# Kernel tuning notes

Hardware: AMD Instinct MI355X
Metric: run time of the kernel (lower is better)

The kernel has to match this reference:

```python
import jax, jax.numpy as jnp
import numpy as np

H = 20  # hidden_size


def _cell(x, h, c, Wih, Whh, b):
    # PyTorch LSTM gate order: i, f, g, o ; b = b_ih + b_hh (merged)
    g = x @ Wih.T + h @ Whh.T + b
    i, f, gg, o = jnp.split(g, 4, axis=-1)
    c = jax.nn.sigmoid(f) * c + jax.nn.sigmoid(i) * jnp.tanh(gg)
    h = jax.nn.sigmoid(o) * jnp.tanh(c)
    return h, c


def _run_lstm(seq, h0, c0, params):
    # seq: [B,T,D]; h0,c0: [L,B,H]; params: list of (Wih, Whh, b) per layer
    def step(carry, x_t):
        h, c = carry
        inp = x_t
        hs, cs = [], []
        for l, (Wih, Whh, b) in enumerate(params):
            hl, cl = _cell(inp, h[l], c[l], Wih, Whh, b)
            hs.append(hl); cs.append(cl)
            inp = hl
        h = jnp.stack(hs); c = jnp.stack(cs)
        return (h, c), h[-1]
    (h, c), last_layer_h = jax.lax.scan(step, (h0, c0), jnp.swapaxes(seq, 0, 1))
    return h, c, last_layer_h  # last_layer_h: [T,B,H]


def setup_inputs() -> dict:
    key = jax.random.key(0)
    ks = jax.random.split(key, 32)
    B = 131072
    d = {
        'y_past': jax.random.normal(ks[0], (B, 8, 1), jnp.float32),
        'x_past': jax.random.normal(ks[1], (B, 8, 8), jnp.float32),
        'u_past': jax.random.normal(ks[2], (B, 8, 4), jnp.float32),
        's_past': jax.random.normal(ks[3], (B, 8, 3), jnp.float32),
        'u_future': jax.random.normal(ks[4], (B, 4, 4), jnp.float32),
    }
    s = 0.1
    # lstm (input_size=16), 2 layers
    d['Wih1_0'] = jax.random.normal(ks[5], (4 * H, 16), jnp.float32) * s
    d['Whh1_0'] = jax.random.normal(ks[6], (4 * H, H), jnp.float32) * s
    d['b1_0'] = jax.random.normal(ks[7], (4 * H,), jnp.float32) * s
    d['Wih1_1'] = jax.random.normal(ks[8], (4 * H, H), jnp.float32) * s
    d['Whh1_1'] = jax.random.normal(ks[9], (4 * H, H), jnp.float32) * s
    d['b1_1'] = jax.random.normal(ks[10], (4 * H,), jnp.float32) * s
    # lstm_2 (input_size=u_size=4), 2 layers
    d['Wih2_0'] = jax.random.normal(ks[11], (4 * H, 4), jnp.float32) * s
    d['Whh2_0'] = jax.random.normal(ks[12], (4 * H, H), jnp.float32) * s
    d['b2_0'] = jax.random.normal(ks[13], (4 * H,), jnp.float32) * s
    d['Wih2_1'] = jax.random.normal(ks[14], (4 * H, H), jnp.float32) * s
    d['Whh2_1'] = jax.random.normal(ks[15], (4 * H, H), jnp.float32) * s
    d['b2_1'] = jax.random.normal(ks[16], (4 * H,), jnp.float32) * s
    # FCNN 20 -> 10 -> 10 -> 1
    d['fW1'] = jax.random.normal(ks[17], (10, 20), jnp.float32) * s
    d['fb1'] = jax.random.normal(ks[18], (10,), jnp.float32) * s
    d['fW2'] = jax.random.normal(ks[19], (10, 10), jnp.float32) * s
    d['fb2'] = jax.random.normal(ks[20], (10,), jnp.float32) * s
    d['fW3'] = jax.random.normal(ks[21], (1, 10), jnp.float32) * s
    d['fb3'] = jax.random.normal(ks[22], (1,), jnp.float32) * s
    return d


def reference(y_past, x_past, u_past, s_past, u_future,
              Wih1_0, Whh1_0, b1_0, Wih1_1, Whh1_1, b1_1,
              Wih2_0, Whh2_0, b2_0, Wih2_1, Whh2_1, b2_1,
              fW1, fb1, fW2, fb2, fW3, fb3):
    inp = jnp.concatenate([y_past, x_past, u_past, s_past], axis=2)  # [B,T,16]
    B = inp.shape[0]
    h0 = jnp.zeros((2, B, H), inp.dtype)
    c0 = jnp.zeros((2, B, H), inp.dtype)
    # encoder LSTM over lookback window (state carried, outputs discarded)
    h, c, _ = _run_lstm(inp, h0, c0, [(Wih1_0, Whh1_0, b1_0), (Wih1_1, Whh1_1, b1_1)])
    # decoder LSTM over lookahead, collecting last-layer h each step
    _, _, hs = _run_lstm(u_future, h, c, [(Wih2_0, Whh2_0, b2_0), (Wih2_1, Whh2_1, b2_1)])
    # FCNN head applied per step: [T2,B,H] -> [T2,B,1]
    z = jax.nn.relu(hs @ fW1.T + fb1)
    z = jax.nn.relu(z @ fW2.T + fb2)
    z = z @ fW3.T + fb3
    return jnp.swapaxes(z, 0, 1)  # [B, lookahead, 1]
```

## Files before the change

### kernel.cpp

```cpp
#include <hip/hip_runtime.h>
#include <utility>

#define HH 20

typedef float v2f __attribute__((ext_vector_type(2)));

__device__ __forceinline__ float fast_rcp(float x) { return __builtin_amdgcn_rcpf(x); }
__device__ __forceinline__ float fsigmoid(float x) { return fast_rcp(1.0f + __expf(-x)); }
__device__ __forceinline__ float ftanh(float x) {
    float e = __expf(2.0f * x);
    return 1.0f - 2.0f * fast_rcp(e + 1.0f);
}
__device__ __forceinline__ float pswap(float v) {
    return __int_as_float(__builtin_amdgcn_mov_dpp(__float_as_int(v), 0xB1, 0xF, 0xF, true));
}
__device__ __forceinline__ v2f fma2(v2f a, v2f b, v2f c) {
#if __has_builtin(__builtin_elementwise_fma)
    return __builtin_elementwise_fma(a, b, c);
#else
    v2f r; r.x = fmaf(a.x, b.x, c.x); r.y = fmaf(a.y, b.y, c.y); return r;
#endif
}

constexpr int BLK16 = 20 * 16 + 4;
constexpr int BLK20 = 20 * 20 + 4;
constexpr int BLK4  = 20 * 4 + 4;

constexpr int W_Wih1_0 = 0;
constexpr int W_Whh1_0 = W_Wih1_0 + 4 * BLK16;
constexpr int W_b1_0   = W_Whh1_0 + 4 * BLK20;
constexpr int W_Wih1_1 = W_b1_0 + 80;
constexpr int W_Whh1_1 = W_Wih1_1 + 4 * BLK20;
constexpr int W_b1_1   = W_Whh1_1 + 4 * BLK20;
constexpr int W_Wih2_0 = W_b1_1 + 80;
constexpr int W_Whh2_0 = W_Wih2_0 + 4 * BLK4;
constexpr int W_b2_0   = W_Whh2_0 + 4 * BLK20;
constexpr int W_Wih2_1 = W_b2_0 + 80;
constexpr int W_Whh2_1 = W_Wih2_1 + 4 * BLK20;
constexpr int W_b2_1   = W_Whh2_1 + 4 * BLK20;
constexpr int W_fW1    = W_b2_1 + 80;
constexpr int W_fb1    = W_fW1 + 200;
constexpr int W_fW2    = W_fb1 + 12;
constexpr int W_fb2    = W_fW2 + 100;
constexpr int W_fW3    = W_fb2 + 12;
constexpr int W_fb3    = W_fW3 + 10;
constexpr int LDS_TOT  = W_fb3 + 2;

template <int IN, size_t U, size_t K>
__device__ __forceinline__ void row2_k(const float (&sm)[LDS_TOT], int rb,
                                       const v2f (&v)[IN], v2f& a) {
    float4 w = *(const float4*)&sm[rb + (int)(U * IN + 4 * K)];
    v2f w0 = {w.x, w.x}, w1 = {w.y, w.y}, w2 = {w.z, w.z}, w3 = {w.w, w.w};
    a = fma2(w0, v[4 * K + 0], a);
    a = fma2(w1, v[4 * K + 1], a);
    a = fma2(w2, v[4 * K + 2], a);
    a = fma2(w3, v[4 * K + 3], a);
}
template <int IN, size_t U, size_t... K>
__device__ __forceinline__ void row2(const float (&sm)[LDS_TOT], int rb,
                                     const v2f (&v)[IN], v2f& a, std::index_sequence<K...>) {
    (row2_k<IN, U, K>(sm, rb, v, a), ...);
}

template <int IN, size_t U>
__device__ __forceinline__ void unit2(const float (&sm)[LDS_TOT], int s, float m, float mm1,
                                      int wihA, int wihB, int whhA, int whhB, int bA, int bB,
                                      const v2f (&xp)[IN], const v2f (&hp)[HH],
                                      float (&c_own)[HH], float (&hn)[HH]) {
    float bAv = sm[bA + (int)U];
    float bBv = sm[bB + (int)U];
    v2f aA = {bAv, bAv};
    v2f aB = {bBv, bBv};
    row2<IN, U>(sm, wihA, xp, aA, std::make_index_sequence<IN / 4>{});
    row2<IN, U>(sm, wihB, xp, aB, std::make_index_sequence<IN / 4>{});
    row2<HH, U>(sm, whhA, hp, aA, std::make_index_sequence<HH / 4>{});
    row2<HH, U>(sm, whhB, hp, aB, std::make_index_sequence<HH / 4>{});
    float Ao = fsigmoid(aA.x), At = fsigmoid(aA.y);
    float Bo = fmaf(m, fsigmoid(m * aB.x), -mm1);
    float Bt = fmaf(m, fsigmoid(m * aB.y), -mm1);
    float rA = pswap(At);
    float rB = pswap(Bt);
    float sf = s ? rB : Bo;
    float si = s ? rA : Ao;
    float tg = s ? Bo : rB;
    float so = s ? Ao : rA;
    float cn = fmaf(sf, c_own[U], si * tg);
    c_own[U] = cn;
    hn[U] = so * ftanh(cn);
}

template <int WIH, int WHH, int BOFF, int IN, int BLK, size_t... U, size_t... K>
__device__ __forceinline__ void cell_impl(const float (&sm)[LDS_TOT], int wb, int s,
                                          float m, float mm1,
                                          const float (&x_own)[IN],
                                          float (&h_own)[HH], float (&c_own)[HH],
                                          std::index_sequence<U...>, std::index_sequence<K...>) {
    v2f xp[IN], hp[HH];
    ((xp[K].x = x_own[K], xp[K].y = pswap(x_own[K])), ...);
    ((hp[U].x = h_own[U], hp[U].y = pswap(h_own[U])), ...);
    const int gA = s ? 3 : 0, gB = s ? 2 : 1;
    int wihA = wb + WIH + gA * BLK;
    int wihB = wb + WIH + gB * BLK;
    int whhA = wb + WHH + gA * BLK20;
    int whhB = wb + WHH + gB * BLK20;
    int bA = wb + BOFF + gA * 20;
    int bB = wb + BOFF + gB * 20;
    float hn[HH];
    (unit2<IN, U>(sm, s, m, mm1, wihA, wihB, whhA, whhB, bA, bB,
                  xp, hp, c_own, hn), ...);
    ((h_own[U] = hn[U]), ...);
}

template <int WIH, int WHH, int BOFF, int IN, int BLK>
__device__ __forceinline__ void cell(const float (&sm)[LDS_TOT], int wb, int s,
                                     float m, float mm1, const float (&x_own)[IN],
                                     float (&h_own)[HH], float (&c_own)[HH]) {
    cell_impl<WIH, WHH, BOFF, IN, BLK>(sm, wb, s, m, mm1, x_own, h_own, c_own,
                                       std::make_index_sequence<HH>{},
                                       std::make_index_sequence<IN>{});
}

template <int WOFF, size_t J, int LD, int NV, size_t... K>
__device__ __forceinline__ float mlp_dot(const float (&sm)[LDS_TOT], int wb, const float (&v)[NV],
                                         float a, std::index_sequence<K...>) {
    ((a = fmaf(sm[wb + WOFF + (int)(J * LD + K)], v[K], a)), ...);
    return a;
}
template <size_t... J>
__device__ __forceinline__ void mlp_l1(const float (&sm)[LDS_TOT], int wb,
                                       const float (&h)[HH], float (&z)[10], std::index_sequence<J...>) {
    ((z[J] = fmaxf(mlp_dot<W_fW1, J, HH>(sm, wb, h, sm[wb + W_fb1 + (int)J],
                                         std::make_index_sequence<HH>{}), 0.f)), ...);
}
template <size_t... J>
__device__ __forceinline__ void mlp_l2(const float (&sm)[LDS_TOT], int wb,
                                       const float (&z1)[10], float (&z2)[10], std::index_sequence<J...>) {
    ((z2[J] = fmaxf(mlp_dot<W_fW2, J, 10>(sm, wb, z1, sm[wb + W_fb2 + (int)J],
                                          std::make_index_sequence<10>{}), 0.f)), ...);
}

__global__ void __launch_bounds__(256, 2) lstm_ar_kernel(
    const float* __restrict__ y_past, const float* __restrict__ x_past,
    const float* __restrict__ u_past, const float* __restrict__ s_past,
    const float* __restrict__ u_future,
    const float* __restrict__ Wih1_0, const float* __restrict__ Whh1_0, const float* __restrict__ b1_0,
    const float* __restrict__ Wih1_1, const float* __restrict__ Whh1_1, const float* __restrict__ b1_1,
    const float* __restrict__ Wih2_0, const float* __restrict__ Whh2_0, const float* __restrict__ b2_0,
    const float* __restrict__ Wih2_1, const float* __restrict__ Whh2_1, const float* __restrict__ b2_1,
    const float* __restrict__ fW1, const float* __restrict__ fb1,
    const float* __restrict__ fW2, const float* __restrict__ fb2,
    const float* __restrict__ fW3, const float* __restrict__ fb3,
    float* __restrict__ out, int B) {
    __shared__ __align__(16) float smem[LDS_TOT];
    const int tid = threadIdx.x;

    auto stage_w = [&](const float* src, int off, int IN) {
        const int gb = 20 * IN;
        for (int i = tid; i < 4 * gb; i += 256) {
            int g = i / gb;
            smem[off + g * (gb + 4) + (i - g * gb)] = src[i];
        }
    };
    auto stage = [&](const float* src, int off, int n) {
        for (int i = tid; i < n; i += 256) smem[off + i] = src[i];
    };
    stage_w(Wih1_0, W_Wih1_0, 16);
    stage_w(Whh1_0, W_Whh1_0, 20);
    stage(b1_0, W_b1_0, 80);
    stage_w(Wih1_1, W_Wih1_1, 20);
    stage_w(Whh1_1, W_Whh1_1, 20);
    stage(b1_1, W_b1_1, 80);
    stage_w(Wih2_0, W_Wih2_0, 4);
    stage_w(Whh2_0, W_Whh2_0, 20);
    stage(b2_0, W_b2_0, 80);
    stage_w(Wih2_1, W_Wih2_1, 20);
    stage_w(Whh2_1, W_Whh2_1, 20);
    stage(b2_1, W_b2_1, 80);
    stage(fW1, W_fW1, 200);
    stage(fb1, W_fb1, 10);
    stage(fW2, W_fW2, 100);
    stage(fb2, W_fb2, 10);
    stage(fW3, W_fW3, 10);
    stage(fb3, W_fb3, 1);
    __syncthreads();

    const int s = tid & 1;
    const int e = blockIdx.x * 256 + tid;
    if (e >= B) return;

    const float m   = s ? 2.0f : 1.0f;
    const float mm1 = m - 1.0f;

    float h0[HH], c0[HH], h1[HH], c1[HH];
    {
        auto zero = [&](auto... u) {
            ((h0[u] = 0.f, c0[u] = 0.f, h1[u] = 0.f, c1[u] = 0.f), ...);
        };
        zero(0, 1, 2, 3, 4, 5, 6, 7, 8, 9, 10, 11, 12, 13, 14, 15, 16, 17, 18, 19);
    }

    int wb = 0;

#pragma clang loop unroll(disable)
    for (int t = 0; t < 8; ++t) {
        asm volatile("" : "+s"(wb));
        float x[16];
        x[0] = y_past[e * 8 + t];
        {
            const float4* p = (const float4*)(x_past + (size_t)(e * 8 + t) * 8);
            float4 a0 = p[0], a1 = p[1];
            x[1] = a0.x; x[2] = a0.y; x[3] = a0.z; x[4] = a0.w;
            x[5] = a1.x; x[6] = a1.y; x[7] = a1.z; x[8] = a1.w;
        }
        {
            const float4* p = (const float4*)(u_past + (size_t)(e * 8 + t) * 4);
            float4 a0 = p[0];
            x[9] = a0.x; x[10] = a0.y; x[11] = a0.z; x[12] = a0.w;
        }
        {
            const float* p = s_past + (size_t)(e * 8 + t) * 3;
            x[13] = p[0]; x[14] = p[1]; x[15] = p[2];
        }
        cell<W_Wih1_0, W_Whh1_0, W_b1_0, 16, BLK16>(smem, wb, s, m, mm1, x, h0, c0);
        cell<W_Wih1_1, W_Whh1_1, W_b1_1, HH, BLK20>(smem, wb, s, m, mm1, h0, h1, c1);
    }

#pragma clang loop unroll(disable)
    for (int t = 0; t < 4; ++t) {
        asm volatile("" : "+s"(wb));
        float x[4];
        {
            const float4* p = (const float4*)(u_future + (size_t)(e * 4 + t) * 4);
            float4 a0 = p[0];
            x[0] = a0.x; x[1] = a0.y; x[2] = a0.z; x[3] = a0.w;
        }
        cell<W_Wih2_0, W_Whh2_0, W_b2_0, 4, BLK4>(smem, wb, s, m, mm1, x, h0, c0);
        cell<W_Wih2_1, W_Whh2_1, W_b2_1, HH, BLK20>(smem, wb, s, m, mm1, h0, h1, c1);

        float z1[10], z2[10];
        mlp_l1(smem, wb, h1, z1, std::make_index_sequence<10>{});
        mlp_l2(smem, wb, z1, z2, std::make_index_sequence<10>{});
        float o = mlp_dot<W_fW3, 0, 10>(smem, wb, z2, smem[wb + W_fb3],
                                        std::make_index_sequence<10>{});
        out[e * 4 + t] = o;
    }
}

extern "C" void kernel_launch(void* const* d_in, const int* in_sizes, int n_in,
                              void* d_out, int out_size, void* d_ws, size_t ws_size,
                              hipStream_t stream) {
    (void)n_in; (void)d_ws; (void)ws_size;
    const float* y_past   = (const float*)d_in[0];
    const float* x_past   = (const float*)d_in[1];
    const float* u_past   = (const float*)d_in[2];
    const float* s_past   = (const float*)d_in[3];
    const float* u_future = (const float*)d_in[4];
    const float* Wih1_0 = (const float*)d_in[5];
    const float* Whh1_0 = (const float*)d_in[6];
    const float* b1_0   = (const float*)d_in[7];
    const float* Wih1_1 = (const float*)d_in[8];
    const float* Whh1_1 = (const float*)d_in[9];
    const float* b1_1   = (const float*)d_in[10];
    const float* Wih2_0 = (const float*)d_in[11];
    const float* Whh2_0 = (const float*)d_in[12];
    const float* b2_0   = (const float*)d_in[13];
    const float* Wih2_1 = (const float*)d_in[14];
    const float* Whh2_1 = (const float*)d_in[15];
    const float* b2_1   = (const float*)d_in[16];
    const float* fW1 = (const float*)d_in[17];
    const float* fb1 = (const float*)d_in[18];
    const float* fW2 = (const float*)d_in[19];
    const float* fb2 = (const float*)d_in[20];
    const float* fW3 = (const float*)d_in[21];
    const float* fb3 = (const float*)d_in[22];
    float* out = (float*)d_out;

    int B = in_sizes[0] / 8;
    (void)out_size;

    dim3 block(256);
    dim3 grid((B + 255) / 256);
    lstm_ar_kernel<<<grid, block, 0, stream>>>(
        y_past, x_past, u_past, s_past, u_future,
        Wih1_0, Whh1_0, b1_0, Wih1_1, Whh1_1, b1_1,
        Wih2_0, Whh2_0, b2_0, Wih2_1, Whh2_1, b2_1,
        fW1, fb1, fW2, fb2, fW3, fb3, out, B);
}
```

Measured before the change: 562.6 us.

## Read LSTM weights from global scalar loads instead of LDS with lane-pair split

Drops LDS staging of all weights and the lane-pair scheme where two adjacent threads split gate work via DPP swaps. Each thread now computes all four gates for its own batch element, loading weights straight from global memory at wave-uniform addresses that the compiler can issue as scalar loads. Dot products use packed pairs along the input dimension, reduced at the end. This removes LDS traffic and cross-lane shuffles but doubles per-thread gate arithmetic and depends on scalar cache bandwidth.

Measured after the change: 855.5 us. 1.52x slower.

```diff
diff --git a/kernel.cpp b/kernel.cpp
--- a/kernel.cpp
+++ b/kernel.cpp
@@ -11,9 +11,7 @@
     float e = __expf(2.0f * x);
     return 1.0f - 2.0f * fast_rcp(e + 1.0f);
 }
-__device__ __forceinline__ float pswap(float v) {
-    return __int_as_float(__builtin_amdgcn_mov_dpp(__float_as_int(v), 0xB1, 0xF, 0xF, true));
-}
+
 __device__ __forceinline__ v2f fma2(v2f a, v2f b, v2f c) {
 #if __has_builtin(__builtin_elementwise_fma)
     return __builtin_elementwise_fma(a, b, c);
@@ -22,121 +20,87 @@
 #endif
 }
 
-constexpr int BLK16 = 20 * 16 + 4;
-constexpr int BLK20 = 20 * 20 + 4;
-constexpr int BLK4  = 20 * 4 + 4;
-
-constexpr int W_Wih1_0 = 0;
-constexpr int W_Whh1_0 = W_Wih1_0 + 4 * BLK16;
-constexpr int W_b1_0   = W_Whh1_0 + 4 * BLK20;
-constexpr int W_Wih1_1 = W_b1_0 + 80;
-constexpr int W_Whh1_1 = W_Wih1_1 + 4 * BLK20;
-constexpr int W_b1_1   = W_Whh1_1 + 4 * BLK20;
-constexpr int W_Wih2_0 = W_b1_1 + 80;
-constexpr int W_Whh2_0 = W_Wih2_0 + 4 * BLK4;
-constexpr int W_b2_0   = W_Whh2_0 + 4 * BLK20;
-constexpr int W_Wih2_1 = W_b2_0 + 80;
-constexpr int W_Whh2_1 = W_Wih2_1 + 4 * BLK20;
-constexpr int W_b2_1   = W_Whh2_1 + 4 * BLK20;
-constexpr int W_fW1    = W_b2_1 + 80;
-constexpr int W_fb1    = W_fW1 + 200;
-constexpr int W_fW2    = W_fb1 + 12;
-constexpr int W_fb2    = W_fW2 + 100;
-constexpr int W_fW3    = W_fb2 + 12;
-constexpr int W_fb3    = W_fW3 + 10;
-constexpr int LDS_TOT  = W_fb3 + 2;
-
-template <int IN, size_t U, size_t K>
-__device__ __forceinline__ void row2_k(const float (&sm)[LDS_TOT], int rb,
-                                       const v2f (&v)[IN], v2f& a) {
-    float4 w = *(const float4*)&sm[rb + (int)(U * IN + 4 * K)];
-    v2f w0 = {w.x, w.x}, w1 = {w.y, w.y}, w2 = {w.z, w.z}, w3 = {w.w, w.w};
-    a = fma2(w0, v[4 * K + 0], a);
-    a = fma2(w1, v[4 * K + 1], a);
-    a = fma2(w2, v[4 * K + 2], a);
-    a = fma2(w3, v[4 * K + 3], a);
-}
-template <int IN, size_t U, size_t... K>
-__device__ __forceinline__ void row2(const float (&sm)[LDS_TOT], int rb,
-                                     const v2f (&v)[IN], v2f& a, std::index_sequence<K...>) {
-    (row2_k<IN, U, K>(sm, rb, v, a), ...);
-}
-
-template <int IN, size_t U>
-__device__ __forceinline__ void unit2(const float (&sm)[LDS_TOT], int s, float m, float mm1,
-                                      int wihA, int wihB, int whhA, int whhB, int bA, int bB,
-                                      const v2f (&xp)[IN], const v2f (&hp)[HH],
-                                      float (&c_own)[HH], float (&hn)[HH]) {
-    float bAv = sm[bA + (int)U];
-    float bBv = sm[bB + (int)U];
-    v2f aA = {bAv, bAv};
-    v2f aB = {bBv, bBv};
-    row2<IN, U>(sm, wihA, xp, aA, std::make_index_sequence<IN / 4>{});
-    row2<IN, U>(sm, wihB, xp, aB, std::make_index_sequence<IN / 4>{});
-    row2<HH, U>(sm, whhA, hp, aA, std::make_index_sequence<HH / 4>{});
-    row2<HH, U>(sm, whhB, hp, aB, std::make_index_sequence<HH / 4>{});
-    float Ao = fsigmoid(aA.x), At = fsigmoid(aA.y);
-    float Bo = fmaf(m, fsigmoid(m * aB.x), -mm1);
-    float Bt = fmaf(m, fsigmoid(m * aB.y), -mm1);
-    float rA = pswap(At);
-    float rB = pswap(Bt);
-    float sf = s ? rB : Bo;
-    float si = s ? rA : Ao;
-    float tg = s ? Bo : rB;
-    float so = s ? Ao : rA;
-    float cn = fmaf(sf, c_own[U], si * tg);
-    c_own[U] = cn;
+template <int NP, size_t... J>
+__device__ __forceinline__ v2f dot2i(const float* __restrict__ W, int base,
+                                     const v2f (&p)[NP], v2f acc, std::index_sequence<J...>) {
+    ((acc = fma2(*(const v2f*)(W + base + 2 * (int)J), p[J], acc)), ...);
+    return acc;
+}
+template <int NP>
+__device__ __forceinline__ v2f dot2(const float* __restrict__ W, int base,
+                                    const v2f (&p)[NP], v2f acc) {
+    return dot2i<NP>(W, base, p, acc, std::make_index_sequence<NP>{});
+}
+
+template <int N, size_t... J>
+__device__ __forceinline__ void mkpairs_i(const float (&a)[N], v2f (&p)[N / 2],
+                                          std::index_sequence<J...>) {
+    ((p[J] = v2f{a[2 * J], a[2 * J + 1]}), ...);
+}
+template <int N>
+__device__ __forceinline__ void mkpairs(const float (&a)[N], v2f (&p)[N / 2]) {
+    mkpairs_i<N>(a, p, std::make_index_sequence<N / 2>{});
+}
+
+template <int IN, int U>
+__device__ __forceinline__ void unitK(const float* __restrict__ Wih, const float* __restrict__ Whh,
+                                      const float* __restrict__ bb, int z,
+                                      const v2f (&xp)[IN / 2], const v2f (&hp)[HH / 2],
+                                      float (&c)[HH], float (&hn)[HH]) {
+    const v2f zz = {0.f, 0.f};
+    v2f ai = dot2<IN / 2>(Wih, z + (0 * HH + U) * IN, xp, zz);
+    v2f af = dot2<IN / 2>(Wih, z + (1 * HH + U) * IN, xp, zz);
+    v2f ag = dot2<IN / 2>(Wih, z + (2 * HH + U) * IN, xp, zz);
+    v2f ao = dot2<IN / 2>(Wih, z + (3 * HH + U) * IN, xp, zz);
+    ai = dot2<HH / 2>(Whh, z + (0 * HH + U) * HH, hp, ai);
+    af = dot2<HH / 2>(Whh, z + (1 * HH + U) * HH, hp, af);
+    ag = dot2<HH / 2>(Whh, z + (2 * HH + U) * HH, hp, ag);
+    ao = dot2<HH / 2>(Whh, z + (3 * HH + U) * HH, hp, ao);
+    float gi = ai.x + ai.y + bb[z + 0 * HH + U];
+    float gf = af.x + af.y + bb[z + 1 * HH + U];
+    float gg = ag.x + ag.y + bb[z + 2 * HH + U];
+    float go = ao.x + ao.y + bb[z + 3 * HH + U];
+    float si = fsigmoid(gi);
+    float sf = fsigmoid(gf);
+    float so = fsigmoid(go);
+    float tg = ftanh(gg);
+    float cn = fmaf(sf, c[U], si * tg);
+    c[U] = cn;
     hn[U] = so * ftanh(cn);
 }
 
-template <int WIH, int WHH, int BOFF, int IN, int BLK, size_t... U, size_t... K>
-__device__ __forceinline__ void cell_impl(const float (&sm)[LDS_TOT], int wb, int s,
-                                          float m, float mm1,
-                                          const float (&x_own)[IN],
-                                          float (&h_own)[HH], float (&c_own)[HH],
-                                          std::index_sequence<U...>, std::index_sequence<K...>) {
-    v2f xp[IN], hp[HH];
-    ((xp[K].x = x_own[K], xp[K].y = pswap(x_own[K])), ...);
-    ((hp[U].x = h_own[U], hp[U].y = pswap(h_own[U])), ...);
-    const int gA = s ? 3 : 0, gB = s ? 2 : 1;
-    int wihA = wb + WIH + gA * BLK;
-    int wihB = wb + WIH + gB * BLK;
-    int whhA = wb + WHH + gA * BLK20;
-    int whhB = wb + WHH + gB * BLK20;
-    int bA = wb + BOFF + gA * 20;
-    int bB = wb + BOFF + gB * 20;
+template <int IN, size_t... U>
+__device__ __forceinline__ void cellK_u(const float* __restrict__ Wih, const float* __restrict__ Whh,
+                                        const float* __restrict__ bb, int z,
+                                        const v2f (&xp)[IN / 2], float (&h)[HH], float (&c)[HH],
+                                        std::index_sequence<U...>) {
+    v2f hp[HH / 2];
+    mkpairs<HH>(h, hp);
     float hn[HH];
-    (unit2<IN, U>(sm, s, m, mm1, wihA, wihB, whhA, whhB, bA, bB,
-                  xp, hp, c_own, hn), ...);
-    ((h_own[U] = hn[U]), ...);
-}
-
-template <int WIH, int WHH, int BOFF, int IN, int BLK>
-__device__ __forceinline__ void cell(const float (&sm)[LDS_TOT], int wb, int s,
-                                     float m, float mm1, const float (&x_own)[IN],
-                                     float (&h_own)[HH], float (&c_own)[HH]) {
-    cell_impl<WIH, WHH, BOFF, IN, BLK>(sm, wb, s, m, mm1, x_own, h_own, c_own,
-                                       std::make_index_sequence<HH>{},
-                                       std::make_index_sequence<IN>{});
-}
-
-template <int WOFF, size_t J, int LD, int NV, size_t... K>
-__device__ __forceinline__ float mlp_dot(const float (&sm)[LDS_TOT], int wb, const float (&v)[NV],
-                                         float a, std::index_sequence<K...>) {
-    ((a = fmaf(sm[wb + WOFF + (int)(J * LD + K)], v[K], a)), ...);
-    return a;
-}
-template <size_t... J>
-__device__ __forceinline__ void mlp_l1(const float (&sm)[LDS_TOT], int wb,
-                                       const float (&h)[HH], float (&z)[10], std::index_sequence<J...>) {
-    ((z[J] = fmaxf(mlp_dot<W_fW1, J, HH>(sm, wb, h, sm[wb + W_fb1 + (int)J],
-                                         std::make_index_sequence<HH>{}), 0.f)), ...);
-}
-template <size_t... J>
-__device__ __forceinline__ void mlp_l2(const float (&sm)[LDS_TOT], int wb,
-                                       const float (&z1)[10], float (&z2)[10], std::index_sequence<J...>) {
-    ((z2[J] = fmaxf(mlp_dot<W_fW2, J, 10>(sm, wb, z1, sm[wb + W_fb2 + (int)J],
-                                          std::make_index_sequence<10>{}), 0.f)), ...);
+    (unitK<IN, (int)U>(Wih, Whh, bb, z, xp, hp, c, hn), ...);
+    ((h[U] = hn[U]), ...);
+}
+template <int IN>
+__device__ __forceinline__ void cellK(const float* __restrict__ Wih, const float* __restrict__ Whh,
+                                      const float* __restrict__ bb, int z,
+                                      const float (&x)[IN], float (&h)[HH], float (&c)[HH]) {
+    v2f xp[IN / 2];
+    mkpairs<IN>(x, xp);
+    cellK_u<IN>(Wih, Whh, bb, z, xp, h, c, std::make_index_sequence<HH>{});
+}
+
+template <int NP>
+__device__ __forceinline__ float rowdot(const float* __restrict__ W, int base,
+                                        const v2f (&p)[NP], float b) {
+    const v2f zz = {0.f, 0.f};
+    v2f a = dot2<NP>(W, base, p, zz);
+    return a.x + a.y + b;
+}
+template <int NP, int LD, size_t... J>
+__device__ __forceinline__ void mlp_layer(const float* __restrict__ W, const float* __restrict__ bv,
+                                          int z, const v2f (&p)[NP], float (&o)[10],
+                                          std::index_sequence<J...>) {
+    ((o[J] = fmaxf(rowdot<NP>(W, z + (int)J * LD, p, bv[z + (int)J]), 0.f)), ...);
 }
 
 __global__ void __launch_bounds__(256, 2) lstm_ar_kernel(
@@ -151,45 +115,8 @@
     const float* __restrict__ fW2, const float* __restrict__ fb2,
     const float* __restrict__ fW3, const float* __restrict__ fb3,
     float* __restrict__ out, int B) {
-    __shared__ __align__(16) float smem[LDS_TOT];
-    const int tid = threadIdx.x;
-
-    auto stage_w = [&](const float* src, int off, int IN) {
-        const int gb = 20 * IN;
-        for (int i = tid; i < 4 * gb; i += 256) {
-            int g = i / gb;
-            smem[off + g * (gb + 4) + (i - g * gb)] = src[i];
-        }
-    };
-    auto stage = [&](const float* src, int off, int n) {
-        for (int i = tid; i < n; i += 256) smem[off + i] = src[i];
-    };
-    stage_w(Wih1_0, W_Wih1_0, 16);
-    stage_w(Whh1_0, W_Whh1_0, 20);
-    stage(b1_0, W_b1_0, 80);
-    stage_w(Wih1_1, W_Wih1_1, 20);
-    stage_w(Whh1_1, W_Whh1_1, 20);
-    stage(b1_1, W_b1_1, 80);
-    stage_w(Wih2_0, W_Wih2_0, 4);
-    stage_w(Whh2_0, W_Whh2_0, 20);
-    stage(b2_0, W_b2_0, 80);
-    stage_w(Wih2_1, W_Wih2_1, 20);
-    stage_w(Whh2_1, W_Whh2_1, 20);
-    stage(b2_1, W_b2_1, 80);
-    stage(fW1, W_fW1, 200);
-    stage(fb1, W_fb1, 10);
-    stage(fW2, W_fW2, 100);
-    stage(fb2, W_fb2, 10);
-    stage(fW3, W_fW3, 10);
-    stage(fb3, W_fb3, 1);
-    __syncthreads();
-
-    const int s = tid & 1;
-    const int e = blockIdx.x * 256 + tid;
+    const int e = blockIdx.x * 256 + threadIdx.x;
     if (e >= B) return;
-
-    const float m   = s ? 2.0f : 1.0f;
-    const float mm1 = m - 1.0f;
 
     float h0[HH], c0[HH], h1[HH], c1[HH];
     {
@@ -199,11 +126,10 @@
         zero(0, 1, 2, 3, 4, 5, 6, 7, 8, 9, 10, 11, 12, 13, 14, 15, 16, 17, 18, 19);
     }
 
-    int wb = 0;
-
 #pragma clang loop unroll(disable)
     for (int t = 0; t < 8; ++t) {
-        asm volatile("" : "+s"(wb));
+        int z = 0;
+        asm volatile("" : "+s"(z));
         float x[16];
         x[0] = y_past[e * 8 + t];
         {
@@ -221,27 +147,33 @@
             const float* p = s_past + (size_t)(e * 8 + t) * 3;
             x[13] = p[0]; x[14] = p[1]; x[15] = p[2];
         }
-        cell<W_Wih1_0, W_Whh1_0, W_b1_0, 16, BLK16>(smem, wb, s, m, mm1, x, h0, c0);
-        cell<W_Wih1_1, W_Whh1_1, W_b1_1, HH, BLK20>(smem, wb, s, m, mm1, h0, h1, c1);
+        cellK<16>(Wih1_0, Whh1_0, b1_0, z, x, h0, c0);
+        cellK<HH>(Wih1_1, Whh1_1, b1_1, z, h0, h1, c1);
     }
 
 #pragma clang loop unroll(disable)
     for (int t = 0; t < 4; ++t) {
-        asm volatile("" : "+s"(wb));
+        int z = 0;
+        asm volatile("" : "+s"(z));
         float x[4];
         {
             const float4* p = (const float4*)(u_future + (size_t)(e * 4 + t) * 4);
             float4 a0 = p[0];
             x[0] = a0.x; x[1] = a0.y; x[2] = a0.z; x[3] = a0.w;
         }
-        cell<W_Wih2_0, W_Whh2_0, W_b2_0, 4, BLK4>(smem, wb, s, m, mm1, x, h0, c0);
-        cell<W_Wih2_1, W_Whh2_1, W_b2_1, HH, BLK20>(smem, wb, s, m, mm1, h0, h1, c1);
-
+        cellK<4>(Wih2_0, Whh2_0, b2_0, z, x, h0, c0);
+        cellK<HH>(Wih2_1, Whh2_1, b2_1, z, h0, h1, c1);
+
+        v2f hp1[HH / 2];
+        mkpairs<HH>(h1, hp1);
         float z1[10], z2[10];
-        mlp_l1(smem, wb, h1, z1, std::make_index_sequence<10>{});
-        mlp_l2(smem, wb, z1, z2, std::make_index_sequence<10>{});
-        float o = mlp_dot<W_fW3, 0, 10>(smem, wb, z2, smem[wb + W_fb3],
-                                        std::make_index_sequence<10>{});
+        mlp_layer<HH / 2, HH>(fW1, fb1, z, hp1, z1, std::make_index_sequence<10>{});
+        v2f zp1[5];
+        mkpairs<10>(z1, zp1);
+        mlp_layer<5, 10>(fW2, fb2, z, zp1, z2, std::make_index_sequence<10>{});
+        v2f zp2[5];
+        mkpairs<10>(z2, zp2);
+        float o = rowdot<5>(fW3, z + 0, zp2, fb3[z + 0]);
         out[e * 4 + t] = o;
     }
 }
```

## Process two batch elements per thread to reuse LDS weight loads

Applied to the files above, without the earlier changes.

Each thread now carries two independent sequences (e0 and e0+B/2) packed in v2f registers, so every LDS weight load feeds twice as many packed FMAs. The MLP head is also rewritten to use packed fma2 over both elements. The aim is to halve LDS weight traffic per element and improve ILP. In exchange register pressure roughly doubles, the launch bound drops to 128 threads with 1 block per CU, and half as many threads are launched, which lowers occupancy and latency hiding. Odd B would drop the last element.

New measurement: 631.1 us. +12.2%, slower.

```diff
diff --git a/kernel.cpp b/kernel.cpp
--- a/kernel.cpp
+++ b/kernel.cpp
@@ -21,6 +21,8 @@
     v2f r; r.x = fmaf(a.x, b.x, c.x); r.y = fmaf(a.y, b.y, c.y); return r;
 #endif
 }
+__device__ __forceinline__ v2f splat2(float w) { return v2f{w, w}; }
+__device__ __forceinline__ v2f relu2(v2f a) { return v2f{fmaxf(a.x, 0.f), fmaxf(a.y, 0.f)}; }
 
 constexpr int BLK16 = 20 * 16 + 4;
 constexpr int BLK20 = 20 * 20 + 4;
@@ -47,57 +49,78 @@
 constexpr int LDS_TOT  = W_fb3 + 2;
 
 template <int IN, size_t U, size_t K>
-__device__ __forceinline__ void row2_k(const float (&sm)[LDS_TOT], int rb,
-                                       const v2f (&v)[IN], v2f& a) {
+__device__ __forceinline__ void row2x_k(const float (&sm)[LDS_TOT], int rb,
+                                        const v2f (&p0)[IN], const v2f (&p1)[IN],
+                                        v2f& a0, v2f& a1) {
     float4 w = *(const float4*)&sm[rb + (int)(U * IN + 4 * K)];
-    v2f w0 = {w.x, w.x}, w1 = {w.y, w.y}, w2 = {w.z, w.z}, w3 = {w.w, w.w};
-    a = fma2(w0, v[4 * K + 0], a);
-    a = fma2(w1, v[4 * K + 1], a);
-    a = fma2(w2, v[4 * K + 2], a);
-    a = fma2(w3, v[4 * K + 3], a);
+    v2f w0 = splat2(w.x), w1 = splat2(w.y), w2 = splat2(w.z), w3 = splat2(w.w);
+    a0 = fma2(w0, p0[4 * K + 0], a0);  a1 = fma2(w0, p1[4 * K + 0], a1);
+    a0 = fma2(w1, p0[4 * K + 1], a0);  a1 = fma2(w1, p1[4 * K + 1], a1);
+    a0 = fma2(w2, p0[4 * K + 2], a0);  a1 = fma2(w2, p1[4 * K + 2], a1);
+    a0 = fma2(w3, p0[4 * K + 3], a0);  a1 = fma2(w3, p1[4 * K + 3], a1);
 }
 template <int IN, size_t U, size_t... K>
-__device__ __forceinline__ void row2(const float (&sm)[LDS_TOT], int rb,
-                                     const v2f (&v)[IN], v2f& a, std::index_sequence<K...>) {
-    (row2_k<IN, U, K>(sm, rb, v, a), ...);
+__device__ __forceinline__ void row2x(const float (&sm)[LDS_TOT], int rb,
+                                      const v2f (&p0)[IN], const v2f (&p1)[IN],
+                                      v2f& a0, v2f& a1, std::index_sequence<K...>) {
+    (row2x_k<IN, U, K>(sm, rb, p0, p1, a0, a1), ...);
 }
 
 template <int IN, size_t U>
-__device__ __forceinline__ void unit2(const float (&sm)[LDS_TOT], int s, float m, float mm1,
-                                      int wihA, int wihB, int whhA, int whhB, int bA, int bB,
-                                      const v2f (&xp)[IN], const v2f (&hp)[HH],
-                                      float (&c_own)[HH], float (&hn)[HH]) {
+__device__ __forceinline__ void unit2x(const float (&sm)[LDS_TOT], int s, float m, float mm1,
+                                       int wihA, int wihB, int whhA, int whhB, int bA, int bB,
+                                       const v2f (&xp0)[IN], const v2f (&xp1)[IN],
+                                       const v2f (&hp0)[HH], const v2f (&hp1)[HH],
+                                       v2f (&c_own)[HH], v2f (&hn)[HH]) {
     float bAv = sm[bA + (int)U];
     float bBv = sm[bB + (int)U];
-    v2f aA = {bAv, bAv};
-    v2f aB = {bBv, bBv};
-    row2<IN, U>(sm, wihA, xp, aA, std::make_index_sequence<IN / 4>{});
-    row2<IN, U>(sm, wihB, xp, aB, std::make_index_sequence<IN / 4>{});
-    row2<HH, U>(sm, whhA, hp, aA, std::make_index_sequence<HH / 4>{});
-    row2<HH, U>(sm, whhB, hp, aB, std::make_index_sequence<HH / 4>{});
-    float Ao = fsigmoid(aA.x), At = fsigmoid(aA.y);
-    float Bo = fmaf(m, fsigmoid(m * aB.x), -mm1);
-    float Bt = fmaf(m, fsigmoid(m * aB.y), -mm1);
-    float rA = pswap(At);
-    float rB = pswap(Bt);
-    float sf = s ? rB : Bo;
-    float si = s ? rA : Ao;
-    float tg = s ? Bo : rB;
-    float so = s ? Ao : rA;
-    float cn = fmaf(sf, c_own[U], si * tg);
-    c_own[U] = cn;
-    hn[U] = so * ftanh(cn);
+    v2f aA0 = splat2(bAv), aA1 = splat2(bAv);
+    v2f aB0 = splat2(bBv), aB1 = splat2(bBv);
+    row2x<IN, U>(sm, wihA, xp0, xp1, aA0, aA1, std::make_index_sequence<IN / 4>{});
+    row2x<IN, U>(sm, wihB, xp0, xp1, aB0, aB1, std::make_index_sequence<IN / 4>{});
+    row2x<HH, U>(sm, whhA, hp0, hp1, aA0, aA1, std::make_index_sequence<HH / 4>{});
+    row2x<HH, U>(sm, whhB, hp0, hp1, aB0, aB1, std::make_index_sequence<HH / 4>{});
+    float cn0, cn1;
+    {
+        float Ao = fsigmoid(aA0.x), At = fsigmoid(aA0.y);
+        float Bo = fmaf(m, fsigmoid(m * aB0.x), -mm1);
+        float Bt = fmaf(m, fsigmoid(m * aB0.y), -mm1);
+        float rA = pswap(At);
+        float rB = pswap(Bt);
+        float sf = s ? rB : Bo;
+        float si = s ? rA : Ao;
+        float tg = s ? Bo : rB;
+        float so = s ? Ao : rA;
+        cn0 = fmaf(sf, c_own[U].x, si * tg);
+        hn[U].x = so * ftanh(cn0);
+    }
+    {
+        float Ao = fsigmoid(aA1.x), At = fsigmoid(aA1.y);
+        float Bo = fmaf(m, fsigmoid(m * aB1.x), -mm1);
+        float Bt = fmaf(m, fsigmoid(m * aB1.y), -mm1);
+        float rA = pswap(At);
+        float rB = pswap(Bt);
+        float sf = s ? rB : Bo;
+        float si = s ? rA : Ao;
+        float tg = s ? Bo : rB;
+        float so = s ? Ao : rA;
+        cn1 = fmaf(sf, c_own[U].y, si * tg);
+        hn[U].y = so * ftanh(cn1);
+    }
+    c_own[U] = v2f{cn0, cn1};
 }
 
 template <int WIH, int WHH, int BOFF, int IN, int BLK, size_t... U, size_t... K>
 __device__ __forceinline__ void cell_impl(const float (&sm)[LDS_TOT], int wb, int s,
                                           float m, float mm1,
-                                          const float (&x_own)[IN],
-                                          float (&h_own)[HH], float (&c_own)[HH],
+                                          const v2f (&xo)[IN],
+                                          v2f (&h_own)[HH], v2f (&c_own)[HH],
                                           std::index_sequence<U...>, std::index_sequence<K...>) {
-    v2f xp[IN], hp[HH];
-    ((xp[K].x = x_own[K], xp[K].y = pswap(x_own[K])), ...);
-    ((hp[U].x = h_own[U], hp[U].y = pswap(h_own[U])), ...);
+    v2f xp0[IN], xp1[IN], hp0[HH], hp1[HH];
+    ((xp0[K] = v2f{xo[K].x, pswap(xo[K].x)},
+      xp1[K] = v2f{xo[K].y, pswap(xo[K].y)}), ...);
+    ((hp0[U] = v2f{h_own[U].x, pswap(h_own[U].x)},
+      hp1[U] = v2f{h_own[U].y, pswap(h_own[U].y)}), ...);
     const int gA = s ? 3 : 0, gB = s ? 2 : 1;
     int wihA = wb + WIH + gA * BLK;
     int wihB = wb + WIH + gB * BLK;
@@ -105,41 +128,41 @@
     int whhB = wb + WHH + gB * BLK20;
     int bA = wb + BOFF + gA * 20;
     int bB = wb + BOFF + gB * 20;
-    float hn[HH];
-    (unit2<IN, U>(sm, s, m, mm1, wihA, wihB, whhA, whhB, bA, bB,
-                  xp, hp, c_own, hn), ...);
+    v2f hn[HH];
+    (unit2x<IN, U>(sm, s, m, mm1, wihA, wihB, whhA, whhB, bA, bB,
+                   xp0, xp1, hp0, hp1, c_own, hn), ...);
     ((h_own[U] = hn[U]), ...);
 }
 
 template <int WIH, int WHH, int BOFF, int IN, int BLK>
 __device__ __forceinline__ void cell(const float (&sm)[LDS_TOT], int wb, int s,
-                                     float m, float mm1, const float (&x_own)[IN],
-                                     float (&h_own)[HH], float (&c_own)[HH]) {
-    cell_impl<WIH, WHH, BOFF, IN, BLK>(sm, wb, s, m, mm1, x_own, h_own, c_own,
+                                     float m, float mm1, const v2f (&xo)[IN],
+                                     v2f (&h_own)[HH], v2f (&c_own)[HH]) {
+    cell_impl<WIH, WHH, BOFF, IN, BLK>(sm, wb, s, m, mm1, xo, h_own, c_own,
                                        std::make_index_sequence<HH>{},
                                        std::make_index_sequence<IN>{});
 }
 
-template <int WOFF, size_t J, int LD, int NV, size_t... K>
-__device__ __forceinline__ float mlp_dot(const float (&sm)[LDS_TOT], int wb, const float (&v)[NV],
-                                         float a, std::index_sequence<K...>) {
-    ((a = fmaf(sm[wb + WOFF + (int)(J * LD + K)], v[K], a)), ...);
-    return a;
-}
-template <size_t... J>
-__device__ __forceinline__ void mlp_l1(const float (&sm)[LDS_TOT], int wb,
-                                       const float (&h)[HH], float (&z)[10], std::index_sequence<J...>) {
-    ((z[J] = fmaxf(mlp_dot<W_fW1, J, HH>(sm, wb, h, sm[wb + W_fb1 + (int)J],
-                                         std::make_index_sequence<HH>{}), 0.f)), ...);
-}
-template <size_t... J>
-__device__ __forceinline__ void mlp_l2(const float (&sm)[LDS_TOT], int wb,
-                                       const float (&z1)[10], float (&z2)[10], std::index_sequence<J...>) {
-    ((z2[J] = fmaxf(mlp_dot<W_fW2, J, 10>(sm, wb, z1, sm[wb + W_fb2 + (int)J],
-                                          std::make_index_sequence<10>{}), 0.f)), ...);
-}
-
-__global__ void __launch_bounds__(256, 2) lstm_ar_kernel(
+template <int NF, size_t... K>
+__device__ __forceinline__ v2f vdot_i(const float (&sm)[LDS_TOT], int base,
+                                      const v2f (&p)[NF], v2f acc, std::index_sequence<K...>) {
+    ((acc = fma2(splat2(sm[base + (int)K]), p[K], acc)), ...);
+    return acc;
+}
+template <int NF>
+__device__ __forceinline__ v2f vdot(const float (&sm)[LDS_TOT], int base,
+                                    const v2f (&p)[NF], v2f acc) {
+    return vdot_i<NF>(sm, base, p, acc, std::make_index_sequence<NF>{});
+}
+template <int WOFF, int BOFF, int NF, int LD, size_t... J>
+__device__ __forceinline__ void mlp_layer(const float (&sm)[LDS_TOT], int z,
+                                          const v2f (&p)[NF], v2f (&o)[10],
+                                          std::index_sequence<J...>) {
+    ((o[J] = relu2(vdot<NF>(sm, z + WOFF + (int)J * LD, p,
+                            splat2(sm[z + BOFF + (int)J])))), ...);
+}
+
+__global__ void __launch_bounds__(128, 1) lstm_ar_kernel(
     const float* __restrict__ y_past, const float* __restrict__ x_past,
     const float* __restrict__ u_past, const float* __restrict__ s_past,
     const float* __restrict__ u_future,
@@ -156,13 +179,13 @@
 
     auto stage_w = [&](const float* src, int off, int IN) {
         const int gb = 20 * IN;
-        for (int i = tid; i < 4 * gb; i += 256) {
+        for (int i = tid; i < 4 * gb; i += 128) {
             int g = i / gb;
             smem[off + g * (gb + 4) + (i - g * gb)] = src[i];
         }
     };
     auto stage = [&](const float* src, int off, int n) {
-        for (int i = tid; i < n; i += 256) smem[off + i] = src[i];
+        for (int i = tid; i < n; i += 128) smem[off + i] = src[i];
     };
     stage_w(Wih1_0, W_Wih1_0, 16);
     stage_w(Whh1_0, W_Whh1_0, 20);
@@ -185,16 +208,20 @@
     __syncthreads();
 
     const int s = tid & 1;
-    const int e = blockIdx.x * 256 + tid;
-    if (e >= B) return;
+    const int half = B >> 1;
+    const int g = blockIdx.x * 128 + tid;
+    if (g >= half) return;
+    const int e0 = g;
+    const int e1 = g + half;
 
     const float m   = s ? 2.0f : 1.0f;
     const float mm1 = m - 1.0f;
 
-    float h0[HH], c0[HH], h1[HH], c1[HH];
+    v2f h0[HH], c0[HH], h1[HH], c1[HH];
     {
         auto zero = [&](auto... u) {
-            ((h0[u] = 0.f, c0[u] = 0.f, h1[u] = 0.f, c1[u] = 0.f), ...);
+            ((h0[u] = v2f{0.f, 0.f}, c0[u] = v2f{0.f, 0.f},
+              h1[u] = v2f{0.f, 0.f}, c1[u] = v2f{0.f, 0.f}), ...);
         };
         zero(0, 1, 2, 3, 4, 5, 6, 7, 8, 9, 10, 11, 12, 13, 14, 15, 16, 17, 18, 19);
     }
@@ -204,22 +231,34 @@
 #pragma clang loop unroll(disable)
     for (int t = 0; t < 8; ++t) {
         asm volatile("" : "+s"(wb));
-        float x[16];
-        x[0] = y_past[e * 8 + t];
-        {
-            const float4* p = (const float4*)(x_past + (size_t)(e * 8 + t) * 8);
-            float4 a0 = p[0], a1 = p[1];
-            x[1] = a0.x; x[2] = a0.y; x[3] = a0.z; x[4] = a0.w;
-            x[5] = a1.x; x[6] = a1.y; x[7] = a1.z; x[8] = a1.w;
-        }
-        {
-            const float4* p = (const float4*)(u_past + (size_t)(e * 8 + t) * 4);
-            float4 a0 = p[0];
-            x[9] = a0.x; x[10] = a0.y; x[11] = a0.z; x[12] = a0.w;
-        }
-        {
-            const float* p = s_past + (size_t)(e * 8 + t) * 3;
-            x[13] = p[0]; x[14] = p[1]; x[15] = p[2];
+        v2f x[16];
+        {
+            float a = y_past[e0 * 8 + t];
+            float b = y_past[e1 * 8 + t];
+            x[0] = v2f{a, b};
+        }
+        {
+            const float4* pa = (const float4*)(x_past + (size_t)(e0 * 8 + t) * 8);
+            const float4* pb = (const float4*)(x_past + (size_t)(e1 * 8 + t) * 8);
+            float4 a0 = pa[0], a1 = pa[1], b0 = pb[0], b1 = pb[1];
+            x[1] = v2f{a0.x, b0.x}; x[2] = v2f{a0.y, b0.y};
+            x[3] = v2f{a0.z, b0.z}; x[4] = v2f{a0.w, b0.w};
+            x[5] = v2f{a1.x, b1.x}; x[6] = v2f{a1.y, b1.y};
+            x[7] = v2f{a1.z, b1.z}; x[8] = v2f{a1.w, b1.w};
+        }
+        {
+            const float4* pa = (const float4*)(u_past + (size_t)(e0 * 8 + t) * 4);
+            const float4* pb = (const float4*)(u_past + (size_t)(e1 * 8 + t) * 4);
+            float4 a0 = pa[0], b0 = pb[0];
+            x[9]  = v2f{a0.x, b0.x}; x[10] = v2f{a0.y, b0.y};
+            x[11] = v2f{a0.z, b0.z}; x[12] = v2f{a0.w, b0.w};
+        }
+        {
+            const float* pa = s_past + (size_t)(e0 * 8 + t) * 3;
+            const float* pb = s_past + (size_t)(e1 * 8 + t) * 3;
+            x[13] = v2f{pa[0], pb[0]};
+            x[14] = v2f{pa[1], pb[1]};
+            x[15] = v2f{pa[2], pb[2]};
         }
         cell<W_Wih1_0, W_Whh1_0, W_b1_0, 16, BLK16>(smem, wb, s, m, mm1, x, h0, c0);
         cell<W_Wih1_1, W_Whh1_1, W_b1_1, HH, BLK20>(smem, wb, s, m, mm1, h0, h1, c1);
@@ -228,21 +267,23 @@
 #pragma clang loop unroll(disable)
     for (int t = 0; t < 4; ++t) {
         asm volatile("" : "+s"(wb));
-        float x[4];
-        {
-            const float4* p = (const float4*)(u_future + (size_t)(e * 4 + t) * 4);
-            float4 a0 = p[0];
-            x[0] = a0.x; x[1] = a0.y; x[2] = a0.z; x[3] = a0.w;
+        v2f x[4];
+        {
+            const float4* pa = (const float4*)(u_future + (size_t)(e0 * 4 + t) * 4);
+            const float4* pb = (const float4*)(u_future + (size_t)(e1 * 4 + t) * 4);
+            float4 a0 = pa[0], b0 = pb[0];
+            x[0] = v2f{a0.x, b0.x}; x[1] = v2f{a0.y, b0.y};
+            x[2] = v2f{a0.z, b0.z}; x[3] = v2f{a0.w, b0.w};
         }
         cell<W_Wih2_0, W_Whh2_0, W_b2_0, 4, BLK4>(smem, wb, s, m, mm1, x, h0, c0);
         cell<W_Wih2_1, W_Whh2_1, W_b2_1, HH, BLK20>(smem, wb, s, m, mm1, h0, h1, c1);
 
-        float z1[10], z2[10];
-        mlp_l1(smem, wb, h1, z1, std::make_index_sequence<10>{});
-        mlp_l2(smem, wb, z1, z2, std::make_index_sequence<10>{});
-        float o = mlp_dot<W_fW3, 0, 10>(smem, wb, z2, smem[wb + W_fb3],
-                                        std::make_index_sequence<10>{});
-        out[e * 4 + t] = o;
+        v2f z1[10], z2[10];
+        mlp_layer<W_fW1, W_fb1, HH, HH>(smem, wb, h1, z1, std::make_index_sequence<10>{});
+        mlp_layer<W_fW2, W_fb2, 10, 10>(smem, wb, z1, z2, std::make_index_sequence<10>{});
+        v2f o = vdot<10>(smem, wb + W_fW3, z2, splat2(smem[wb + W_fb3]));
+        out[e0 * 4 + t] = o.x;
+        out[e1 * 4 + t] = o.y;
     }
 }
 
@@ -278,8 +319,9 @@
     int B = in_sizes[0] / 8;
     (void)out_size;
 
-    dim3 block(256);
-    dim3 grid((B + 255) / 256);
+    int nthreads = B / 2;
+    dim3 block(128);
+    dim3 grid((nthreads + 127) / 128);
     lstm_ar_kernel<<<grid, block, 0, stream>>>(
         y_past, x_past, u_past, s_past, u_future,
         Wih1_0, Whh1_0, b1_0, Wih1_1, Whh1_1, b1_1,
```

## Split LSTM gate computation across lane quads instead of lane pairs

Applied to the files above, without the earlier changes.

Each lane in a group of four now computes one gate (i, f, g or o) for its own and its three neighbours' batch elements, using DPP quad permutes to exchange inputs and activations. Before, pairs of lanes each computed two gates. The weight-row LDS reads per lane drop from two gate rows to one, which reduces LDS traffic and float4 loads per FMA. In exchange there are more DPP moves (three per input instead of one) and more select instructions to route the gate values.

Measured after the change: 587.9 us. +4.5%, slower.

```diff
diff --git a/kernel.cpp b/kernel.cpp
--- a/kernel.cpp
+++ b/kernel.cpp
@@ -11,8 +11,12 @@
     float e = __expf(2.0f * x);
     return 1.0f - 2.0f * fast_rcp(e + 1.0f);
 }
-__device__ __forceinline__ float pswap(float v) {
-    return __int_as_float(__builtin_amdgcn_mov_dpp(__float_as_int(v), 0xB1, 0xF, 0xF, true));
+constexpr int XOR1 = 0xB1;
+constexpr int XOR2 = 0x4E;
+constexpr int XOR3 = 0x1B;
+template <int CTRL>
+__device__ __forceinline__ float qdpp(float v) {
+    return __int_as_float(__builtin_amdgcn_mov_dpp(__float_as_int(v), CTRL, 0xF, 0xF, true));
 }
 __device__ __forceinline__ v2f fma2(v2f a, v2f b, v2f c) {
 #if __has_builtin(__builtin_elementwise_fma)
@@ -21,6 +25,7 @@
     v2f r; r.x = fmaf(a.x, b.x, c.x); r.y = fmaf(a.y, b.y, c.y); return r;
 #endif
 }
+__device__ __forceinline__ v2f splat2(float w) { return v2f{w, w}; }
 
 constexpr int BLK16 = 20 * 16 + 4;
 constexpr int BLK20 = 20 * 20 + 4;
@@ -47,75 +52,74 @@
 constexpr int LDS_TOT  = W_fb3 + 2;
 
 template <int IN, size_t U, size_t K>
-__device__ __forceinline__ void row2_k(const float (&sm)[LDS_TOT], int rb,
-                                       const v2f (&v)[IN], v2f& a) {
+__device__ __forceinline__ void rowq_k(const float (&sm)[LDS_TOT], int rb,
+                                       const v2f (&p01)[IN], const v2f (&p23)[IN],
+                                       v2f& a01, v2f& a23) {
     float4 w = *(const float4*)&sm[rb + (int)(U * IN + 4 * K)];
-    v2f w0 = {w.x, w.x}, w1 = {w.y, w.y}, w2 = {w.z, w.z}, w3 = {w.w, w.w};
-    a = fma2(w0, v[4 * K + 0], a);
-    a = fma2(w1, v[4 * K + 1], a);
-    a = fma2(w2, v[4 * K + 2], a);
-    a = fma2(w3, v[4 * K + 3], a);
+    v2f w0 = splat2(w.x), w1 = splat2(w.y), w2 = splat2(w.z), w3 = splat2(w.w);
+    a01 = fma2(w0, p01[4 * K + 0], a01);  a23 = fma2(w0, p23[4 * K + 0], a23);
+    a01 = fma2(w1, p01[4 * K + 1], a01);  a23 = fma2(w1, p23[4 * K + 1], a23);
+    a01 = fma2(w2, p01[4 * K + 2], a01);  a23 = fma2(w2, p23[4 * K + 2], a23);
+    a01 = fma2(w3, p01[4 * K + 3], a01);  a23 = fma2(w3, p23[4 * K + 3], a23);
 }
 template <int IN, size_t U, size_t... K>
-__device__ __forceinline__ void row2(const float (&sm)[LDS_TOT], int rb,
-                                     const v2f (&v)[IN], v2f& a, std::index_sequence<K...>) {
-    (row2_k<IN, U, K>(sm, rb, v, a), ...);
+__device__ __forceinline__ void rowq(const float (&sm)[LDS_TOT], int rb,
+                                     const v2f (&p01)[IN], const v2f (&p23)[IN],
+                                     v2f& a01, v2f& a23, std::index_sequence<K...>) {
+    (rowq_k<IN, U, K>(sm, rb, p01, p23, a01, a23), ...);
 }
 
 template <int IN, size_t U>
-__device__ __forceinline__ void unit2(const float (&sm)[LDS_TOT], int s, float m, float mm1,
-                                      int wihA, int wihB, int whhA, int whhB, int bA, int bB,
-                                      const v2f (&xp)[IN], const v2f (&hp)[HH],
-                                      float (&c_own)[HH], float (&hn)[HH]) {
-    float bAv = sm[bA + (int)U];
-    float bBv = sm[bB + (int)U];
-    v2f aA = {bAv, bAv};
-    v2f aB = {bBv, bBv};
-    row2<IN, U>(sm, wihA, xp, aA, std::make_index_sequence<IN / 4>{});
-    row2<IN, U>(sm, wihB, xp, aB, std::make_index_sequence<IN / 4>{});
-    row2<HH, U>(sm, whhA, hp, aA, std::make_index_sequence<HH / 4>{});
-    row2<HH, U>(sm, whhB, hp, aB, std::make_index_sequence<HH / 4>{});
-    float Ao = fsigmoid(aA.x), At = fsigmoid(aA.y);
-    float Bo = fmaf(m, fsigmoid(m * aB.x), -mm1);
-    float Bt = fmaf(m, fsigmoid(m * aB.y), -mm1);
-    float rA = pswap(At);
-    float rB = pswap(Bt);
-    float sf = s ? rB : Bo;
-    float si = s ? rA : Ao;
-    float tg = s ? Bo : rB;
-    float so = s ? Ao : rA;
-    float cn = fmaf(sf, c_own[U], si * tg);
-    c_own[U] = cn;
+__device__ __forceinline__ void unitq(const float (&sm)[LDS_TOT], bool q0, bool q1,
+                                      float m, float mm1, int rih, int rhh, int rb,
+                                      const v2f (&xp01)[IN], const v2f (&xp23)[IN],
+                                      const v2f (&hp01)[HH], const v2f (&hp23)[HH],
+                                      float (&c)[HH], float (&hn)[HH]) {
+    float bv = sm[rb + (int)U];
+    v2f a01 = splat2(bv), a23 = splat2(bv);
+    rowq<IN, U>(sm, rih, xp01, xp23, a01, a23, std::make_index_sequence<IN / 4>{});
+    rowq<HH, U>(sm, rhh, hp01, hp23, a01, a23, std::make_index_sequence<HH / 4>{});
+    float act0 = fmaf(m, fsigmoid(m * a01.x), -mm1);
+    float act1 = fmaf(m, fsigmoid(m * a01.y), -mm1);
+    float act2 = fmaf(m, fsigmoid(m * a23.x), -mm1);
+    float act3 = fmaf(m, fsigmoid(m * a23.y), -mm1);
+    float c0 = act0;
+    float c1 = qdpp<XOR1>(act1);
+    float c2 = qdpp<XOR2>(act2);
+    float c3 = qdpp<XOR3>(act3);
+    float u0 = q0 ? c1 : c0, u1 = q0 ? c0 : c1, u2 = q0 ? c3 : c2, u3 = q0 ? c2 : c3;
+    float si = q1 ? u2 : u0, sf = q1 ? u3 : u1, tg = q1 ? u0 : u2, so = q1 ? u1 : u3;
+    float cn = fmaf(sf, c[U], si * tg);
+    c[U] = cn;
     hn[U] = so * ftanh(cn);
 }
 
 template <int WIH, int WHH, int BOFF, int IN, int BLK, size_t... U, size_t... K>
-__device__ __forceinline__ void cell_impl(const float (&sm)[LDS_TOT], int wb, int s,
-                                          float m, float mm1,
-                                          const float (&x_own)[IN],
-                                          float (&h_own)[HH], float (&c_own)[HH],
+__device__ __forceinline__ void cell_impl(const float (&sm)[LDS_TOT], int wb, int q,
+                                          bool q0, bool q1, float m, float mm1,
+                                          const float (&x)[IN],
+                                          float (&h)[HH], float (&c)[HH],
                                           std::index_sequence<U...>, std::index_sequence<K...>) {
-    v2f xp[IN], hp[HH];
-    ((xp[K].x = x_own[K], xp[K].y = pswap(x_own[K])), ...);
-    ((hp[U].x = h_own[U], hp[U].y = pswap(h_own[U])), ...);
-    const int gA = s ? 3 : 0, gB = s ? 2 : 1;
-    int wihA = wb + WIH + gA * BLK;
-    int wihB = wb + WIH + gB * BLK;
-    int whhA = wb + WHH + gA * BLK20;
-    int whhB = wb + WHH + gB * BLK20;
-    int bA = wb + BOFF + gA * 20;
-    int bB = wb + BOFF + gB * 20;
+    v2f xp01[IN], xp23[IN], hp01[HH], hp23[HH];
+    ((xp01[K] = v2f{x[K], qdpp<XOR1>(x[K])},
+      xp23[K] = v2f{qdpp<XOR2>(x[K]), qdpp<XOR3>(x[K])}), ...);
+    ((hp01[U] = v2f{h[U], qdpp<XOR1>(h[U])},
+      hp23[U] = v2f{qdpp<XOR2>(h[U]), qdpp<XOR3>(h[U])}), ...);
+    const int rih = wb + WIH + q * BLK;
+    const int rhh = wb + WHH + q * BLK20;
+    const int rb  = wb + BOFF + q * 20;
     float hn[HH];
-    (unit2<IN, U>(sm, s, m, mm1, wihA, wihB, whhA, whhB, bA, bB,
-                  xp, hp, c_own, hn), ...);
-    ((h_own[U] = hn[U]), ...);
+    (unitq<IN, U>(sm, q0, q1, m, mm1, rih, rhh, rb,
+                  xp01, xp23, hp01, hp23, c, hn), ...);
+    ((h[U] = hn[U]), ...);
 }
 
 template <int WIH, int WHH, int BOFF, int IN, int BLK>
-__device__ __forceinline__ void cell(const float (&sm)[LDS_TOT], int wb, int s,
-                                     float m, float mm1, const float (&x_own)[IN],
-                                     float (&h_own)[HH], float (&c_own)[HH]) {
-    cell_impl<WIH, WHH, BOFF, IN, BLK>(sm, wb, s, m, mm1, x_own, h_own, c_own,
+__device__ __forceinline__ void cell(const float (&sm)[LDS_TOT], int wb, int q,
+                                     bool q0, bool q1, float m, float mm1,
+                                     const float (&x)[IN],
+                                     float (&h)[HH], float (&c)[HH]) {
+    cell_impl<WIH, WHH, BOFF, IN, BLK>(sm, wb, q, q0, q1, m, mm1, x, h, c,
                                        std::make_index_sequence<HH>{},
                                        std::make_index_sequence<IN>{});
 }
@@ -184,11 +188,13 @@
     stage(fb3, W_fb3, 1);
     __syncthreads();
 
-    const int s = tid & 1;
+    const int q = tid & 3;
+    const bool q0 = (tid & 1) != 0;
+    const bool q1 = (tid & 2) != 0;
     const int e = blockIdx.x * 256 + tid;
     if (e >= B) return;
 
-    const float m   = s ? 2.0f : 1.0f;
+    const float m   = (q == 2) ? 2.0f : 1.0f;
     const float mm1 = m - 1.0f;
 
     float h0[HH], c0[HH], h1[HH], c1[HH];
@@ -221,8 +227,8 @@
             const float* p = s_past + (size_t)(e * 8 + t) * 3;
             x[13] = p[0]; x[14] = p[1]; x[15] = p[2];
         }
-        cell<W_Wih1_0, W_Whh1_0, W_b1_0, 16, BLK16>(smem, wb, s, m, mm1, x, h0, c0);
-        cell<W_Wih1_1, W_Whh1_1, W_b1_1, HH, BLK20>(smem, wb, s, m, mm1, h0, h1, c1);
+        cell<W_Wih1_0, W_Whh1_0, W_b1_0, 16, BLK16>(smem, wb, q, q0, q1, m, mm1, x, h0, c0);
+        cell<W_Wih1_1, W_Whh1_1, W_b1_1, HH, BLK20>(smem, wb, q, q0, q1, m, mm1, h0, h1, c1);
     }
 
 #pragma clang loop unroll(disable)
@@ -234,8 +240,8 @@
             float4 a0 = p[0];
             x[0] = a0.x; x[1] = a0.y; x[2] = a0.z; x[3] = a0.w;
         }
-        cell<W_Wih2_0, W_Whh2_0, W_b2_0, 4, BLK4>(smem, wb, s, m, mm1, x, h0, c0);
-        cell<W_Wih2_1, W_Whh2_1, W_b2_1, HH, BLK20>(smem, wb, s, m, mm1, h0, h1, c1);
+        cell<W_Wih2_0, W_Whh2_0, W_b2_0, 4, BLK4>(smem, wb, q, q0, q1, m, mm1, x, h0, c0);
+        cell<W_Wih2_1, W_Whh2_1, W_b2_1, HH, BLK20>(smem, wb, q, q0, q1, m, mm1, h0, h1, c1);
 
         float z1[10], z2[10];
         mlp_l1(smem, wb, h1, z1, std::make_index_sequence<10>{});
```
